# Performance work log

Measured on AMD Instinct MI355X. Metric: run time of the kernel, lower is better.

Reference implementation:

```python
import jax, jax.numpy as jnp
import numpy as np

N = 20000          # nodes
E = 320000         # directed edges (self-loops added in reference)
F_IN = 128         # input node features
HEADS = 8
HID = 64           # per-head hidden channels
G = 64             # graphs in the batch
NUM_CLASSES = 10
NEG_SLOPE = 0.2    # PyG GATConv LeakyReLU slope


def _gat_layer(x, src, dst, W, a_src, a_dst, bias, n_nodes):
    """PyG-style GATConv: messages flow src->dst, softmax over incoming edges."""
    H, C = a_src.shape
    h = (x @ W).reshape(n_nodes, H, C)                     # [N,H,C]
    asrc = jnp.einsum('nhc,hc->nh', h, a_src)              # [N,H]
    adst = jnp.einsum('nhc,hc->nh', h, a_dst)              # [N,H]
    e = jax.nn.leaky_relu(asrc[src] + adst[dst], NEG_SLOPE)  # [Etot,H]
    emax = jax.ops.segment_max(e, dst, num_segments=n_nodes)  # [N,H]
    ee = jnp.exp(e - emax[dst])
    denom = jax.ops.segment_sum(ee, dst, num_segments=n_nodes)
    alpha = ee / (denom[dst] + 1e-16)                      # [Etot,H]
    out = jax.ops.segment_sum(h[src] * alpha[:, :, None], dst, num_segments=n_nodes)
    return out.reshape(n_nodes, H * C) + bias


def setup_inputs() -> dict:
    key = jax.random.key(0)
    ks = jax.random.split(key, 10)
    x = jax.random.normal(ks[0], (N, F_IN), jnp.float32)
    edge_index = jax.random.randint(ks[1], (2, E), 0, N, jnp.int32)
    batch = jnp.sort(jax.random.randint(ks[2], (N,), 0, G, jnp.int32))
    # layer 1: F_IN -> HEADS*HID (concat)
    W1 = jax.random.normal(ks[3], (F_IN, HEADS * HID), jnp.float32) / np.float32(np.sqrt(F_IN))
    a_src1 = jax.random.normal(ks[4], (HEADS, HID), jnp.float32) / np.float32(np.sqrt(HID))
    a_dst1 = jax.random.normal(ks[5], (HEADS, HID), jnp.float32) / np.float32(np.sqrt(HID))
    b1 = jnp.zeros((HEADS * HID,), jnp.float32)
    # layer 2: HEADS*HID -> NUM_CLASSES (1 head)
    W2 = jax.random.normal(ks[6], (HEADS * HID, NUM_CLASSES), jnp.float32) / np.float32(np.sqrt(HEADS * HID))
    a_src2 = jax.random.normal(ks[7], (1, NUM_CLASSES), jnp.float32) / np.float32(np.sqrt(NUM_CLASSES))
    a_dst2 = jax.random.normal(ks[8], (1, NUM_CLASSES), jnp.float32) / np.float32(np.sqrt(NUM_CLASSES))
    b2 = jnp.zeros((NUM_CLASSES,), jnp.float32)
    return {"x": x, "edge_index": edge_index, "batch": batch,
            "W1": W1, "a_src1": a_src1, "a_dst1": a_dst1, "b1": b1,
            "W2": W2, "a_src2": a_src2, "a_dst2": a_dst2, "b2": b2}


def reference(x, edge_index, batch, W1, a_src1, a_dst1, b1, W2, a_src2, a_dst2, b2):
    n = x.shape[0]
    loop = jnp.arange(n, dtype=edge_index.dtype)   # add_self_loops=True (PyG default)
    src = jnp.concatenate([edge_index[0], loop])
    dst = jnp.concatenate([edge_index[1], loop])
    h = jax.nn.elu(_gat_layer(x, src, dst, W1, a_src1, a_dst1, b1, n))
    h = _gat_layer(h, src, dst, W2, a_src2, a_dst2, b2, n)
    # PowerMeanAggregation with default p=1.0 == mean pooling per graph
    sums = jax.ops.segment_sum(h, batch, num_segments=G)                    # [G,NC]
    counts = jax.ops.segment_sum(jnp.ones((n, 1), h.dtype), batch, num_segments=G)
    return sums / jnp.maximum(counts, 1.0)
```

## Files before the change

kernel.cpp:

```cpp
#include <hip/hip_runtime.h>
#include <hip/hip_bf16.h>

typedef unsigned short ushort_t;
typedef unsigned int uint_t;
typedef unsigned char uchar_t;

typedef __attribute__((ext_vector_type(8))) short bf16x8;
typedef __attribute__((ext_vector_type(4))) float f32x4;
typedef __attribute__((ext_vector_type(2))) float f32x2;

__device__ __forceinline__ float bf2f(ushort_t u) {
    union { uint_t i; float f; } v; v.i = ((uint_t)u) << 16; return v.f;
}
__device__ __forceinline__ ushort_t f2bf(float f) {
    __hip_bfloat16 h = __float2bfloat16(f);
    ushort_t u; __builtin_memcpy(&u, &h, 2); return u;
}
__device__ __forceinline__ uchar_t f2fp8(float v) {
    int p = __builtin_amdgcn_cvt_pk_fp8_f32(v, v, 0, false);
    return (uchar_t)(p & 0xff);
}
__device__ __forceinline__ float leaky(float v) { return (v > 0.f) ? v : 0.2f * v; }

#define PO_AS1 0
#define PO_AD1 512
#define PO_B1  1024
#define PO_W2  1536
#define PO_AS2 6656
#define PO_AD2 6666
#define PO_B2  6676
#define PTOT   6686

__device__ __forceinline__ bool detect_fp32_local(const ushort_t* __restrict__ xa) {
    __shared__ int cnt;
    if (threadIdx.x == 0) cnt = 0;
    __syncthreads();
    int bad = 0;
    for (int i = threadIdx.x; i < 4096; i += 256) {
        float v = bf2f(xa[i]);
        if (!(fabsf(v) < 1e4f)) bad++;
    }
    if (bad) atomicAdd(&cnt, bad);
    __syncthreads();
    return cnt >= 16;
}

__global__ __launch_bounds__(256) void k_prep(const void* __restrict__ x,
                                              const void* __restrict__ W1,
                                              const void* as1, const void* ad1,
                                              const void* b1, const void* W2,
                                              const void* as2, const void* ad2,
                                              const void* b2,
                                              ushort_t* __restrict__ W1t,
                                              float* __restrict__ prm,
                                              int* __restrict__ deg,
                                              float* __restrict__ gacc,
                                              int* __restrict__ flag, int N) {
    int b = blockIdx.x, t = threadIdx.x;
    if (b < 283) {
        bool isf = detect_fp32_local((const ushort_t*)x);
        if (b == 0 && t == 0) *flag = isf ? 1 : 0;
        if (b < 256) {
            int idx = b * 256 + t;
            int n = idx & 511, k = idx >> 9;
            float v = isf ? ((const float*)W1)[k * 512 + n]
                          : bf2f(((const ushort_t*)W1)[k * 512 + n]);
            W1t[n * 128 + k] = f2bf(v);
        } else {
            int i = (b - 256) * 256 + t;
            if (i < PTOT) {
                const void* src; int off;
                if (i < 512)       { src = as1; off = i; }
                else if (i < 1024) { src = ad1; off = i - 512; }
                else if (i < 1536) { src = b1;  off = i - 1024; }
                else if (i < 6656) { src = W2;  off = i - 1536; }
                else if (i < 6666) { src = as2; off = i - 6656; }
                else if (i < 6676) { src = ad2; off = i - 6666; }
                else               { src = b2;  off = i - 6676; }
                prm[i] = isf ? ((const float*)src)[off] : bf2f(((const ushort_t*)src)[off]);
            }
        }
    } else if (b < 362) {
        int i = (b - 283) * 256 + t;
        if (i < N) deg[i] = 0;
    } else {
        for (int i = t; i < 704; i += 256) gacc[i] = 0.f;
    }
}

__global__ __launch_bounds__(256) void k_gemm_hist(const void* __restrict__ xraw,
                                                   const ushort_t* __restrict__ w1t,
                                                   const float* __restrict__ prm,
                                                   const int* __restrict__ ei,
                                                   const int* __restrict__ flag,
                                                   uchar_t* __restrict__ h1,
                                                   float* __restrict__ asrcf,
                                                   float* __restrict__ adstf,
                                                   int* __restrict__ deg,
                                                   int E, int Etot) {
    int b = blockIdx.x, t = threadIdx.x;
    if (b >= 1250) {
        int e = (b - 1250) * 256 + t;
        if (e < Etot) {
            int dst = (e < E) ? ei[E + e] : (e - E);
            atomicAdd(&deg[dst], 1);
        }
        return;
    }
    int wave = t >> 6, lane = t & 63;
    int m0 = b * 16;
    bool isf = (*flag != 0);
    __shared__ ushort_t sA[16 * 128];
    {
        ushort_t tmp[8];
        if (isf) {
            const float4* x4 = (const float4*)((const float*)xraw + (size_t)m0 * 128);
            float4 f0 = x4[2 * t], f1 = x4[2 * t + 1];
            tmp[0] = f2bf(f0.x); tmp[1] = f2bf(f0.y); tmp[2] = f2bf(f0.z); tmp[3] = f2bf(f0.w);
            tmp[4] = f2bf(f1.x); tmp[5] = f2bf(f1.y); tmp[6] = f2bf(f1.z); tmp[7] = f2bf(f1.w);
        } else {
            const uint4* x4 = (const uint4*)((const ushort_t*)xraw + (size_t)m0 * 128);
            uint4 u = x4[t];
            __builtin_memcpy(tmp, &u, 16);
        }
        *reinterpret_cast<uint4*>(&sA[t * 8]) = *reinterpret_cast<uint4*>(tmp);
    }
    __syncthreads();
    int mr = lane & 15, quad = lane >> 4;
    int n0 = wave * 128;
    f32x4 acc[8];
#pragma unroll
    for (int ct = 0; ct < 8; ++ct) acc[ct] = {0.f, 0.f, 0.f, 0.f};
#pragma unroll
    for (int kk = 0; kk < 4; ++kk) {
        bf16x8 a = *reinterpret_cast<const bf16x8*>(&sA[mr * 128 + quad * 8 + kk * 32]);
#pragma unroll
        for (int ct = 0; ct < 8; ++ct) {
            bf16x8 bb = *reinterpret_cast<const bf16x8*>(
                &w1t[(size_t)(n0 + ct * 16 + mr) * 128 + quad * 8 + kk * 32]);
            acc[ct] = __builtin_amdgcn_mfma_f32_16x16x32_bf16(a, bb, acc[ct], 0, 0, 0);
        }
    }
    int col = lane & 15;
#pragma unroll
    for (int hh = 0; hh < 2; ++hh) {
        float ps[4] = {0.f, 0.f, 0.f, 0.f}, pd[4] = {0.f, 0.f, 0.f, 0.f};
#pragma unroll
        for (int c4 = 0; c4 < 4; ++c4) {
            int ct = hh * 4 + c4;
            int abscol = n0 + ct * 16 + col;
            float asv = prm[PO_AS1 + abscol];
            float adv = prm[PO_AD1 + abscol];
#pragma unroll
            for (int r = 0; r < 4; ++r) {
                h1[(size_t)(m0 + quad * 4 + r) * 512 + abscol] = f2fp8(acc[ct][r]);
                ps[r] += acc[ct][r] * asv;
                pd[r] += acc[ct][r] * adv;
            }
        }
#pragma unroll
        for (int off = 1; off <= 8; off <<= 1) {
#pragma unroll
            for (int r = 0; r < 4; ++r) {
                ps[r] += __shfl_xor(ps[r], off, 64);
                pd[r] += __shfl_xor(pd[r], off, 64);
            }
        }
        if (col == 0) {
            int head = 2 * wave + hh;
#pragma unroll
            for (int r = 0; r < 4; ++r) {
                asrcf[(m0 + quad * 4 + r) * 8 + head] = ps[r];
                adstf[(m0 + quad * 4 + r) * 8 + head] = pd[r];
            }
        }
    }
}

__global__ __launch_bounds__(256) void k_scan(const int* __restrict__ deg,
                                              int* __restrict__ rowptr,
                                              int* __restrict__ cursor, int N) {
    int b = blockIdx.x, t = threadIdx.x;
    int lane = t & 63, wv = t >> 6;
    __shared__ int ws[4], wt[4];
    __shared__ int sbase;
    int limit = b * 256;
    int partial = 0;
    for (int i = t; i < limit; i += 256) partial += deg[i];
#pragma unroll
    for (int off = 32; off; off >>= 1) partial += __shfl_xor(partial, off, 64);
    if (lane == 0) ws[wv] = partial;
    __syncthreads();
    if (t == 0) sbase = ws[0] + ws[1] + ws[2] + ws[3];
    __syncthreads();
    int base = sbase;
    int i = limit + t;
    int v = (i < N) ? deg[i] : 0;
    int inc = v;
#pragma unroll
    for (int off = 1; off < 64; off <<= 1) {
        int u = __shfl_up(inc, off, 64);
        if (lane >= off) inc += u;
    }
    if (lane == 63) wt[wv] = inc;
    __syncthreads();
    int woff = 0;
    for (int w = 0; w < 4; ++w) if (w < wv) woff += wt[w];
    int excl = base + woff + inc - v;
    if (i < N) { rowptr[i + 1] = excl + v; cursor[i] = excl; }
    if (i == 0) rowptr[0] = 0;
}

__global__ __launch_bounds__(256) void k_scatter(const int* __restrict__ ei,
                                                 int* __restrict__ cursor,
                                                 int* __restrict__ csr_src,
                                                 int E, int Etot) {
    int e = blockIdx.x * 256 + threadIdx.x;
    if (e >= Etot) return;
    int src, dst;
    if (e < E) { src = ei[e]; dst = ei[E + e]; } else { src = dst = e - E; }
    int pos = atomicAdd(&cursor[dst], 1);
    csr_src[pos] = src;
}

__global__ __launch_bounds__(256) void k_agg1(const uchar_t* __restrict__ h1,
                                              const float* __restrict__ asrcf,
                                              const float* __restrict__ adstf,
                                              const int* __restrict__ rowptr,
                                              const int* __restrict__ csr_src,
                                              const float* __restrict__ prm,
                                              float* __restrict__ h2,
                                              float* __restrict__ asrc2f,
                                              float* __restrict__ adst2f) {
    int wid = threadIdx.x >> 6;
    int ni = wid >> 1;
    int half = wid & 1;
    int n = blockIdx.x * 2 + ni;
    int lane = threadIdx.x & 63;
    int hh = lane >> 3;
    int cb = lane * 8;
    int start = rowptr[n], end = rowptr[n + 1];
    int deg = end - start;
    int mid = (deg + 1) >> 1;
    int es = start + (half ? mid : 0);
    int ee = half ? end : (start + mid);
    float adh = adstf[n * 8 + hh];
    float a0 = 0.f, a1 = 0.f, a2 = 0.f, a3 = 0.f, a4 = 0.f, a5 = 0.f, a6 = 0.f, a7 = 0.f;
    float den = 0.f;
    for (int base = es; base < ee; base += 64) {
        int m = min(64, ee - base);
        int sIdx = csr_src[base + min(lane, m - 1)];
        for (int g = 0; g < m; g += 8) {
            int s[8]; float lo[8]; uint2 p[8];
#pragma unroll
            for (int j = 0; j < 8; ++j)
                s[j] = __shfl(sIdx, min(g + j, m - 1), 64);
#pragma unroll
            for (int j = 0; j < 8; ++j)
                lo[j] = asrcf[s[j] * 8 + hh];
#pragma unroll
            for (int j = 0; j < 8; ++j)
                p[j] = *reinterpret_cast<const uint2*>(&h1[(size_t)s[j] * 512 + cb]);
#pragma unroll
            for (int j = 0; j < 8; ++j) {
                float we = (g + j < m) ? __expf(leaky(lo[j] + adh)) : 0.f;
                den += we;
                f32x2 q0 = __builtin_amdgcn_cvt_pk_f32_fp8((int)p[j].x, false);
                f32x2 q1 = __builtin_amdgcn_cvt_pk_f32_fp8((int)p[j].x, true);
                f32x2 q2 = __builtin_amdgcn_cvt_pk_f32_fp8((int)p[j].y, false);
                f32x2 q3 = __builtin_amdgcn_cvt_pk_f32_fp8((int)p[j].y, true);
                a0 += we * q0.x; a1 += we * q0.y;
                a2 += we * q1.x; a3 += we * q1.y;
                a4 += we * q2.x; a5 += we * q2.y;
                a6 += we * q3.x; a7 += we * q3.y;
            }
        }
    }
    __shared__ float sred[2][64][9];
    if (half) {
        float* sp = sred[ni][lane];
        sp[0] = a0; sp[1] = a1; sp[2] = a2; sp[3] = a3;
        sp[4] = a4; sp[5] = a5; sp[6] = a6; sp[7] = a7; sp[8] = den;
    }
    __syncthreads();
    if (half) return;
    {
        const float* sp = sred[ni][lane];
        a0 += sp[0]; a1 += sp[1]; a2 += sp[2]; a3 += sp[3];
        a4 += sp[4]; a5 += sp[5]; a6 += sp[6]; a7 += sp[7]; den += sp[8];
    }
    float inv = 1.f / (den + 1e-16f);
    float r[8] = {a0, a1, a2, a3, a4, a5, a6, a7};
    float p2[10];
#pragma unroll
    for (int c = 0; c < 10; ++c) p2[c] = 0.f;
#pragma unroll
    for (int j = 0; j < 8; ++j) {
        float rv = r[j] * inv + prm[PO_B1 + cb + j];
        rv = (rv > 0.f) ? rv : expm1f(rv);
        const float2* wrow = reinterpret_cast<const float2*>(&prm[PO_W2 + (cb + j) * 10]);
        float2 w01 = wrow[0], w23 = wrow[1], w45 = wrow[2], w67 = wrow[3], w89 = wrow[4];
        p2[0] += rv * w01.x; p2[1] += rv * w01.y;
        p2[2] += rv * w23.x; p2[3] += rv * w23.y;
        p2[4] += rv * w45.x; p2[5] += rv * w45.y;
        p2[6] += rv * w67.x; p2[7] += rv * w67.y;
        p2[8] += rv * w89.x; p2[9] += rv * w89.y;
    }
#pragma unroll
    for (int c = 0; c < 10; ++c)
#pragma unroll
        for (int off = 32; off; off >>= 1)
            p2[c] += __shfl_xor(p2[c], off, 64);
    if (lane == 0) {
        float as = 0.f, ad = 0.f;
#pragma unroll
        for (int c = 0; c < 10; ++c) {
            h2[(size_t)n * 16 + c] = p2[c];
            as += p2[c] * prm[PO_AS2 + c];
            ad += p2[c] * prm[PO_AD2 + c];
        }
        asrc2f[n] = as; adst2f[n] = ad;
    }
}

__global__ __launch_bounds__(256) void k_agg2(const float* __restrict__ h2,
                                              const float* __restrict__ asrc2f,
                                              const float* __restrict__ adst2f,
                                              const int* __restrict__ rowptr,
                                              const int* __restrict__ csr_src,
                                              const float* __restrict__ prm,
                                              const int* __restrict__ batch,
                                              float* __restrict__ gacc,
                                              float* __restrict__ gcnt) {
    int t = threadIdx.x;
    int grp = t >> 4, l = t & 15;
    int n = blockIdx.x * 16 + grp;
    int start = rowptr[n], end = rowptr[n + 1];
    float adn = adst2f[n];
    float den = 0.f;
    float oc[10];
#pragma unroll
    for (int c = 0; c < 10; ++c) oc[c] = 0.f;
    for (int e = start + l; e < end; e += 16) {
        int s = csr_src[e];
        float lo = asrc2f[s];
        const float4* hp = reinterpret_cast<const float4*>(&h2[(size_t)s * 16]);
        float4 q0 = hp[0], q1 = hp[1];
        float2 q2 = *reinterpret_cast<const float2*>(&h2[(size_t)s * 16 + 8]);
        float ee = __expf(leaky(lo + adn));
        den += ee;
        oc[0] += ee * q0.x; oc[1] += ee * q0.y; oc[2] += ee * q0.z; oc[3] += ee * q0.w;
        oc[4] += ee * q1.x; oc[5] += ee * q1.y; oc[6] += ee * q1.z; oc[7] += ee * q1.w;
        oc[8] += ee * q2.x; oc[9] += ee * q2.y;
    }
#pragma unroll
    for (int off = 8; off; off >>= 1) {
        den += __shfl_xor(den, off, 64);
#pragma unroll
        for (int c = 0; c < 10; ++c) oc[c] += __shfl_xor(oc[c], off, 64);
    }
    __shared__ float sres[16][12];
    __shared__ int sg[16];
    if (l == 0) {
        float invd = 1.f / (den + 1e-16f);
#pragma unroll
        for (int c = 0; c < 10; ++c) sres[grp][c] = oc[c] * invd + prm[PO_B2 + c];
        sres[grp][10] = 1.f;
        sg[grp] = batch[n];
    }
    __syncthreads();
    if (t < 11) {
        int c = t;
        float run = sres[0][c]; int g = sg[0];
        for (int k = 1; k < 16; ++k) {
            if (sg[k] != g) {
                atomicAdd(c < 10 ? &gacc[g * 10 + c] : &gcnt[g], run);
                g = sg[k]; run = 0.f;
            }
            run += sres[k][c];
        }
        atomicAdd(c < 10 ? &gacc[g * 10 + c] : &gcnt[g], run);
    }
}

__global__ void k_final(const float* __restrict__ gacc,
                        const float* __restrict__ gcnt,
                        const int* __restrict__ flag,
                        void* __restrict__ dout) {
    int g = threadIdx.x;
    if (g >= 64) return;
    bool isf = (*flag != 0);
    float cnt = fmaxf(gcnt[g], 1.f);
    for (int c = 0; c < 10; ++c) {
        float r = gacc[g * 10 + c] / cnt;
        if (isf) ((float*)dout)[g * 10 + c] = r;
        else     ((ushort_t*)dout)[g * 10 + c] = f2bf(r);
    }
}

extern "C" void kernel_launch(void* const* d_in, const int* in_sizes, int n_in,
                              void* d_out, int out_size, void* d_ws, size_t ws_size,
                              hipStream_t stream) {
    const void* x   = d_in[0];
    const int* ei   = (const int*)d_in[1];
    const int* batch= (const int*)d_in[2];
    const void* W1  = d_in[3];
    const void* as1 = d_in[4];
    const void* ad1 = d_in[5];
    const void* b1  = d_in[6];
    const void* W2  = d_in[7];
    const void* as2 = d_in[8];
    const void* ad2 = d_in[9];
    const void* b2  = d_in[10];

    constexpr int N = 20000, E = 320000, Etot = E + N;
    constexpr int histBlocks = (Etot + 255) / 256;

    char* p = (char*)d_ws;
    auto alloc = [&](size_t bytes) {
        char* r = p; p += (bytes + 255) & ~(size_t)255; return r;
    };
    int* flag       = (int*)alloc(256);
    float* prm      = (float*)alloc((size_t)PTOT * 4);
    ushort_t* w1t   = (ushort_t*)alloc(512 * 128 * 2);
    uchar_t* h1     = (uchar_t*)alloc((size_t)N * 512);
    float* asrc1f   = (float*)alloc((size_t)N * 8 * 4);
    float* adst1f   = (float*)alloc((size_t)N * 8 * 4);
    float* asrc2f   = (float*)alloc((size_t)N * 4);
    float* adst2f   = (float*)alloc((size_t)N * 4);
    float* h2       = (float*)alloc((size_t)N * 16 * 4);
    float* gacc     = (float*)alloc((size_t)(64 * 10 + 64) * 4);
    int* deg        = (int*)alloc((size_t)N * 4);
    int* rowptr     = (int*)alloc((size_t)(N + 1) * 4);
    int* cursor     = (int*)alloc((size_t)N * 4);
    int* csr_src    = (int*)alloc((size_t)(Etot + 64) * 4);
    float* gcnt     = gacc + 640;

    k_prep<<<363, 256, 0, stream>>>(x, W1, as1, ad1, b1, W2, as2, ad2, b2,
                                    w1t, prm, deg, gacc, flag, N);
    k_gemm_hist<<<1250 + histBlocks, 256, 0, stream>>>(x, w1t, prm, ei, flag, h1,
                                                       asrc1f, adst1f, deg, E, Etot);
    k_scan<<<(N + 255) / 256, 256, 0, stream>>>(deg, rowptr, cursor, N);
    k_scatter<<<histBlocks, 256, 0, stream>>>(ei, cursor, csr_src, E, Etot);
    k_agg1<<<N / 2, 256, 0, stream>>>(h1, asrc1f, adst1f, rowptr, csr_src, prm,
                                      h2, asrc2f, adst2f);
    k_agg2<<<N / 16, 256, 0, stream>>>(h2, asrc2f, adst2f, rowptr, csr_src, prm,
                                       batch, gacc, gcnt);
    k_final<<<1, 64, 0, stream>>>(gacc, gcnt, flag, d_out);
}
```

Measured before the change: 245.5 us.

## Precompute edge attention weights in scatter, bf16 h2, fuse final into agg2

The scatter kernel now computes exp(leaky(asrc+adst)) for all 8 heads per edge and stores the weights in CSR order, so layer-1 aggregation reads precomputed weights instead of gathering asrc and evaluating exp. The layer-2 features h2 are stored as bf16 to halve gather traffic. The final mean-pooling kernel is folded into agg2 through a last-block-done counter, removing one launch. The scan prefix loop is also unrolled 4x. In exchange, a 10.9 MB weight array is written and read, and h2 loses precision.

```diff
diff --git a/kernel.cpp b/kernel.cpp
--- a/kernel.cpp
+++ b/kernel.cpp
@@ -84,7 +84,7 @@
         int i = (b - 283) * 256 + t;
         if (i < N) deg[i] = 0;
     } else {
-        for (int i = t; i < 704; i += 256) gacc[i] = 0.f;
+        for (int i = t; i < 768; i += 256) gacc[i] = 0.f;
     }
 }
 
@@ -185,8 +185,13 @@
     __shared__ int ws[4], wt[4];
     __shared__ int sbase;
     int limit = b * 256;
-    int partial = 0;
-    for (int i = t; i < limit; i += 256) partial += deg[i];
+    int p0 = 0, p1 = 0, p2 = 0, p3 = 0;
+    int i = t;
+    for (; i + 768 < limit; i += 1024) {
+        p0 += deg[i]; p1 += deg[i + 256]; p2 += deg[i + 512]; p3 += deg[i + 768];
+    }
+    for (; i < limit; i += 256) p0 += deg[i];
+    int partial = (p0 + p1) + (p2 + p3);
 #pragma unroll
     for (int off = 32; off; off >>= 1) partial += __shfl_xor(partial, off, 64);
     if (lane == 0) ws[wv] = partial;
@@ -194,7 +199,7 @@
     if (t == 0) sbase = ws[0] + ws[1] + ws[2] + ws[3];
     __syncthreads();
     int base = sbase;
-    int i = limit + t;
+    i = limit + t;
     int v = (i < N) ? deg[i] : 0;
     int inc = v;
 #pragma unroll
@@ -213,23 +218,41 @@
 
 __global__ __launch_bounds__(256) void k_scatter(const int* __restrict__ ei,
                                                  int* __restrict__ cursor,
+                                                 const float* __restrict__ asrcf,
+                                                 const float* __restrict__ adstf,
                                                  int* __restrict__ csr_src,
+                                                 float* __restrict__ wcsr,
                                                  int E, int Etot) {
     int e = blockIdx.x * 256 + threadIdx.x;
     if (e >= Etot) return;
     int src, dst;
     if (e < E) { src = ei[e]; dst = ei[E + e]; } else { src = dst = e - E; }
     int pos = atomicAdd(&cursor[dst], 1);
-    csr_src[pos] = src;
+    __builtin_nontemporal_store(src, &csr_src[pos]);
+    const float4* ap = (const float4*)&asrcf[(size_t)src * 8];
+    const float4* bp = (const float4*)&adstf[(size_t)dst * 8];
+    float4 a0 = ap[0], a1 = ap[1];
+    float4 b0 = bp[0], b1 = bp[1];
+    f32x4 w0, w1;
+    w0.x = __expf(leaky(a0.x + b0.x));
+    w0.y = __expf(leaky(a0.y + b0.y));
+    w0.z = __expf(leaky(a0.z + b0.z));
+    w0.w = __expf(leaky(a0.w + b0.w));
+    w1.x = __expf(leaky(a1.x + b1.x));
+    w1.y = __expf(leaky(a1.y + b1.y));
+    w1.z = __expf(leaky(a1.z + b1.z));
+    w1.w = __expf(leaky(a1.w + b1.w));
+    f32x4* wp = (f32x4*)&wcsr[(size_t)pos * 8];
+    __builtin_nontemporal_store(w0, wp);
+    __builtin_nontemporal_store(w1, wp + 1);
 }
 
 __global__ __launch_bounds__(256) void k_agg1(const uchar_t* __restrict__ h1,
-                                              const float* __restrict__ asrcf,
-                                              const float* __restrict__ adstf,
                                               const int* __restrict__ rowptr,
                                               const int* __restrict__ csr_src,
+                                              const float* __restrict__ wcsr,
                                               const float* __restrict__ prm,
-                                              float* __restrict__ h2,
+                                              ushort_t* __restrict__ h2,
                                               float* __restrict__ asrc2f,
                                               float* __restrict__ adst2f) {
     int wid = threadIdx.x >> 6;
@@ -244,26 +267,27 @@
     int mid = (deg + 1) >> 1;
     int es = start + (half ? mid : 0);
     int ee = half ? end : (start + mid);
-    float adh = adstf[n * 8 + hh];
     float a0 = 0.f, a1 = 0.f, a2 = 0.f, a3 = 0.f, a4 = 0.f, a5 = 0.f, a6 = 0.f, a7 = 0.f;
     float den = 0.f;
     for (int base = es; base < ee; base += 64) {
         int m = min(64, ee - base);
         int sIdx = csr_src[base + min(lane, m - 1)];
         for (int g = 0; g < m; g += 8) {
-            int s[8]; float lo[8]; uint2 p[8];
+            int s[8]; float w[8]; uint2 p[8];
 #pragma unroll
             for (int j = 0; j < 8; ++j)
                 s[j] = __shfl(sIdx, min(g + j, m - 1), 64);
 #pragma unroll
-            for (int j = 0; j < 8; ++j)
-                lo[j] = asrcf[s[j] * 8 + hh];
+            for (int j = 0; j < 8; ++j) {
+                float wv = wcsr[(size_t)(base + g + j) * 8 + hh];
+                w[j] = (base + g + j < ee) ? wv : 0.f;
+            }
 #pragma unroll
             for (int j = 0; j < 8; ++j)
                 p[j] = *reinterpret_cast<const uint2*>(&h1[(size_t)s[j] * 512 + cb]);
 #pragma unroll
             for (int j = 0; j < 8; ++j) {
-                float we = (g + j < m) ? __expf(leaky(lo[j] + adh)) : 0.f;
+                float we = w[j];
                 den += we;
                 f32x2 q0 = __builtin_amdgcn_cvt_pk_f32_fp8((int)p[j].x, false);
                 f32x2 q1 = __builtin_amdgcn_cvt_pk_f32_fp8((int)p[j].x, true);
@@ -315,7 +339,7 @@
         float as = 0.f, ad = 0.f;
 #pragma unroll
         for (int c = 0; c < 10; ++c) {
-            h2[(size_t)n * 16 + c] = p2[c];
+            h2[(size_t)n * 16 + c] = f2bf(p2[c]);
             as += p2[c] * prm[PO_AS2 + c];
             ad += p2[c] * prm[PO_AD2 + c];
         }
@@ -323,15 +347,18 @@
     }
 }
 
-__global__ __launch_bounds__(256) void k_agg2(const float* __restrict__ h2,
-                                              const float* __restrict__ asrc2f,
-                                              const float* __restrict__ adst2f,
-                                              const int* __restrict__ rowptr,
-                                              const int* __restrict__ csr_src,
-                                              const float* __restrict__ prm,
-                                              const int* __restrict__ batch,
-                                              float* __restrict__ gacc,
-                                              float* __restrict__ gcnt) {
+__global__ __launch_bounds__(256) void k_agg2f(const ushort_t* __restrict__ h2,
+                                               const float* __restrict__ asrc2f,
+                                               const float* __restrict__ adst2f,
+                                               const int* __restrict__ rowptr,
+                                               const int* __restrict__ csr_src,
+                                               const float* __restrict__ prm,
+                                               const int* __restrict__ batch,
+                                               float* __restrict__ gacc,
+                                               float* __restrict__ gcnt,
+                                               int* __restrict__ donecnt,
+                                               const int* __restrict__ flag,
+                                               void* __restrict__ dout) {
     int t = threadIdx.x;
     int grp = t >> 4, l = t & 15;
     int n = blockIdx.x * 16 + grp;
@@ -344,14 +371,16 @@
     for (int e = start + l; e < end; e += 16) {
         int s = csr_src[e];
         float lo = asrc2f[s];
-        const float4* hp = reinterpret_cast<const float4*>(&h2[(size_t)s * 16]);
-        float4 q0 = hp[0], q1 = hp[1];
-        float2 q2 = *reinterpret_cast<const float2*>(&h2[(size_t)s * 16 + 8]);
+        const uint_t* hp = (const uint_t*)(h2 + (size_t)s * 16);
+        uint4 ha = *(const uint4*)hp;
+        uint_t hb = hp[4];
         float ee = __expf(leaky(lo + adn));
         den += ee;
-        oc[0] += ee * q0.x; oc[1] += ee * q0.y; oc[2] += ee * q0.z; oc[3] += ee * q0.w;
-        oc[4] += ee * q1.x; oc[5] += ee * q1.y; oc[6] += ee * q1.z; oc[7] += ee * q1.w;
-        oc[8] += ee * q2.x; oc[9] += ee * q2.y;
+        oc[0] += ee * bf2f(ha.x & 0xffff); oc[1] += ee * bf2f(ha.x >> 16);
+        oc[2] += ee * bf2f(ha.y & 0xffff); oc[3] += ee * bf2f(ha.y >> 16);
+        oc[4] += ee * bf2f(ha.z & 0xffff); oc[5] += ee * bf2f(ha.z >> 16);
+        oc[6] += ee * bf2f(ha.w & 0xffff); oc[7] += ee * bf2f(ha.w >> 16);
+        oc[8] += ee * bf2f(hb & 0xffff);   oc[9] += ee * bf2f(hb >> 16);
     }
 #pragma unroll
     for (int off = 8; off; off >>= 1) {
@@ -381,20 +410,25 @@
         }
         atomicAdd(c < 10 ? &gacc[g * 10 + c] : &gcnt[g], run);
     }
-}
-
-__global__ void k_final(const float* __restrict__ gacc,
-                        const float* __restrict__ gcnt,
-                        const int* __restrict__ flag,
-                        void* __restrict__ dout) {
-    int g = threadIdx.x;
-    if (g >= 64) return;
-    bool isf = (*flag != 0);
-    float cnt = fmaxf(gcnt[g], 1.f);
-    for (int c = 0; c < 10; ++c) {
-        float r = gacc[g * 10 + c] / cnt;
-        if (isf) ((float*)dout)[g * 10 + c] = r;
-        else     ((ushort_t*)dout)[g * 10 + c] = f2bf(r);
+    __syncthreads();
+    __shared__ int slast;
+    if (t == 0) {
+        __threadfence();
+        int d = atomicAdd(donecnt, 1);
+        slast = (d == (int)gridDim.x - 1) ? 1 : 0;
+    }
+    __syncthreads();
+    if (slast && t < 64) {
+        __threadfence();
+        bool isf = (*flag != 0);
+        const volatile float* ga = (const volatile float*)gacc;
+        const volatile float* gc = (const volatile float*)gcnt;
+        float cnt = fmaxf(gc[t], 1.f);
+        for (int c = 0; c < 10; ++c) {
+            float r = ga[t * 10 + c] / cnt;
+            if (isf) ((float*)dout)[t * 10 + c] = r;
+            else     ((ushort_t*)dout)[t * 10 + c] = f2bf(r);
+        }
     }
 }
 
@@ -428,23 +462,25 @@
     float* adst1f   = (float*)alloc((size_t)N * 8 * 4);
     float* asrc2f   = (float*)alloc((size_t)N * 4);
     float* adst2f   = (float*)alloc((size_t)N * 4);
-    float* h2       = (float*)alloc((size_t)N * 16 * 4);
-    float* gacc     = (float*)alloc((size_t)(64 * 10 + 64) * 4);
+    ushort_t* h2    = (ushort_t*)alloc((size_t)N * 16 * 2);
+    float* gacc     = (float*)alloc((size_t)768 * 4);
     int* deg        = (int*)alloc((size_t)N * 4);
     int* rowptr     = (int*)alloc((size_t)(N + 1) * 4);
     int* cursor     = (int*)alloc((size_t)N * 4);
     int* csr_src    = (int*)alloc((size_t)(Etot + 64) * 4);
+    float* wcsr     = (float*)alloc(((size_t)Etot * 8 + 128) * 4);
     float* gcnt     = gacc + 640;
+    int* donecnt    = (int*)(gacc + 704);
 
     k_prep<<<363, 256, 0, stream>>>(x, W1, as1, ad1, b1, W2, as2, ad2, b2,
                                     w1t, prm, deg, gacc, flag, N);
     k_gemm_hist<<<1250 + histBlocks, 256, 0, stream>>>(x, w1t, prm, ei, flag, h1,
                                                        asrc1f, adst1f, deg, E, Etot);
     k_scan<<<(N + 255) / 256, 256, 0, stream>>>(deg, rowptr, cursor, N);
-    k_scatter<<<histBlocks, 256, 0, stream>>>(ei, cursor, csr_src, E, Etot);
-    k_agg1<<<N / 2, 256, 0, stream>>>(h1, asrc1f, adst1f, rowptr, csr_src, prm,
+    k_scatter<<<histBlocks, 256, 0, stream>>>(ei, cursor, asrc1f, adst1f,
+                                              csr_src, wcsr, E, Etot);
+    k_agg1<<<N / 2, 256, 0, stream>>>(h1, rowptr, csr_src, wcsr, prm,
                                       h2, asrc2f, adst2f);
-    k_agg2<<<N / 16, 256, 0, stream>>>(h2, asrc2f, adst2f, rowptr, csr_src, prm,
-                                       batch, gacc, gcnt);
-    k_final<<<1, 64, 0, stream>>>(gacc, gcnt, flag, d_out);
-}
+    k_agg2f<<<N / 16, 256, 0, stream>>>(h2, asrc2f, adst2f, rowptr, csr_src, prm,
+                                        batch, gacc, gcnt, donecnt, flag, d_out);
+}
```

New measurement: 262.9 us. +7.1%, slower.
